# Performance work log

Measured on AMD Instinct MI355X. Metric: run time of the kernel, lower is better.

## Reference

```python
import jax, jax.numpy as jnp
import numpy as np
import math

B, S, D, H, R, DFF = 4, 1024, 1024, 16, 64, 4096

def _layernorm(x, g, b, eps=1e-5):
    m = jnp.mean(x, axis=-1, keepdims=True)
    v = jnp.var(x, axis=-1, keepdims=True)
    return (x - m) / jnp.sqrt(v + eps) * g + b

def setup_inputs() -> dict:
    key = jax.random.key(0)
    ks = jax.random.split(key, 12)
    sc = 0.02
    return {
        "src": jax.random.normal(ks[0], (B, S, D), jnp.float32),
        "in_proj_w": jax.random.normal(ks[1], (3 * D, D), jnp.float32) * sc,
        "in_proj_b": jnp.zeros((3 * D,), jnp.float32),
        "out_proj_w": jax.random.normal(ks[2], (D, D), jnp.float32) * sc,
        "out_proj_b": jnp.zeros((D,), jnp.float32),
        "Qp_w": jax.random.normal(ks[3], (R, D), jnp.float32) * sc,
        "Qp_b": jnp.zeros((R,), jnp.float32),
        "Kp_w": jax.random.normal(ks[4], (R, D), jnp.float32) * sc,
        "Kp_b": jnp.zeros((R,), jnp.float32),
        "Vp_w": jax.random.normal(ks[5], (D, D), jnp.float32) * sc,
        "Vp_b": jnp.zeros((D,), jnp.float32),
        "lam": jnp.float32(0.5),
        "ff1_w": jax.random.normal(ks[6], (DFF, D), jnp.float32) * sc,
        "ff1_b": jnp.zeros((DFF,), jnp.float32),
        "ff2_w": jax.random.normal(ks[7], (D, DFF), jnp.float32) * sc,
        "ff2_b": jnp.zeros((D,), jnp.float32),
        "ln1_g": jnp.ones((D,), jnp.float32),
        "ln1_b": jnp.zeros((D,), jnp.float32),
        "ln2_g": jnp.ones((D,), jnp.float32),
        "ln2_b": jnp.zeros((D,), jnp.float32),
    }

def reference(src, in_proj_w, in_proj_b, out_proj_w, out_proj_b,
              Qp_w, Qp_b, Kp_w, Kp_b, Vp_w, Vp_b, lam,
              ff1_w, ff1_b, ff2_w, ff2_b, ln1_g, ln1_b, ln2_g, ln2_b):
    b, s, d = src.shape
    dh = d // H
    # ---- dense multi-head attention (torch nn.MultiheadAttention, eval) ----
    qkv = src @ in_proj_w.T + in_proj_b            # [B,S,3D]
    q, k, v = jnp.split(qkv, 3, axis=-1)
    q = q.reshape(b, s, H, dh).transpose(0, 2, 1, 3)  # [B,H,S,dh]
    k = k.reshape(b, s, H, dh).transpose(0, 2, 1, 3)
    v = v.reshape(b, s, H, dh).transpose(0, 2, 1, 3)
    scores = jnp.einsum('bhqd,bhkd->bhqk', q, k) / math.sqrt(dh)
    attn = jax.nn.softmax(scores, axis=-1)
    ctx = jnp.einsum('bhqk,bhkd->bhqd', attn, v)
    ctx = ctx.transpose(0, 2, 1, 3).reshape(b, s, d)
    dense_output = ctx @ out_proj_w.T + out_proj_b
    # ---- low-rank top-k sparse attention ----
    Q = src @ Qp_w.T + Qp_b                        # [B,S,R]
    K = src @ Kp_w.T + Kp_b
    V = src @ Vp_w.T + Vp_b                        # [B,S,D]
    QK = jnp.einsum('bqr,bkr->bqk', Q, K) / math.sqrt(R)
    aw = jax.nn.softmax(QK, axis=-1)               # [B,S,S]
    kk = max(1, int(s * 0.2))
    topv, topi = jax.lax.top_k(aw, kk)             # [B,S,kk]
    bi = jnp.arange(b)[:, None, None]
    si = jnp.arange(s)[None, :, None]
    sparse_attn = jnp.zeros_like(aw).at[bi, si, topi].set(topv)
    sparse_attn = sparse_attn / (jnp.sum(sparse_attn, axis=-1, keepdims=True) + 1e-9)
    sparse_output = jnp.einsum('bqk,bkd->bqd', sparse_attn, V)
    # ---- fuse, residual, norm, FFN ----
    sig = jax.nn.sigmoid(lam)
    fused = sig * dense_output + (1.0 - sig) * sparse_output
    x = _layernorm(src + fused, ln1_g, ln1_b)
    ff = jax.nn.relu(x @ ff1_w.T + ff1_b) @ ff2_w.T + ff2_b
    return _layernorm(x + ff, ln2_g, ln2_b)
```

## Files before the change

### kernel.cpp

```cpp
#include <hip/hip_runtime.h>
#include <hip/hip_bf16.h>
#include <math.h>
#include <type_traits>

typedef __hip_bfloat16 bf16;
typedef __attribute__((ext_vector_type(8))) short short8;
typedef __attribute__((ext_vector_type(4))) float f32x4;

#define NB 4
#define NS 1024
#define ND 1024
#define NH 16
#define NDH 64
#define NR 64
#define NDFF 4096
#define NM (NB*NS)
#define NTOPK 204

static __device__ __forceinline__ float b2f(bf16 x) { return __bfloat162float(x); }
static __device__ __forceinline__ bf16  f2b(float x) { return __float2bfloat16(x); }
static __device__ __forceinline__ unsigned short bfbits(float x) {
  bf16 h = __float2bfloat16(x);
  return *reinterpret_cast<unsigned short*>(&h);
}

static __device__ __forceinline__ void gload_lds16(const void* g, void* l) {
  __builtin_amdgcn_global_load_lds(
      (const __attribute__((address_space(1))) void*)g,
      (__attribute__((address_space(3))) void*)l, 16, 0, 0);
}

template<int N> static __device__ __forceinline__ void vm_wait() {
  if constexpr (N == 0)       asm volatile("s_waitcnt vmcnt(0)" ::: "memory");
  else if constexpr (N == 2)  asm volatile("s_waitcnt vmcnt(2)" ::: "memory");
  else if constexpr (N == 4)  asm volatile("s_waitcnt vmcnt(4)" ::: "memory");
  else if constexpr (N == 6)  asm volatile("s_waitcnt vmcnt(6)" ::: "memory");
  else if constexpr (N == 8)  asm volatile("s_waitcnt vmcnt(8)" ::: "memory");
  else static_assert(N == 0, "unsupported vmcnt");
}
static __device__ __forceinline__ void bar() {
  asm volatile("s_barrier" ::: "memory");
}

static __device__ __forceinline__ void ld8(const bf16* p, float* d) {
  const uint4 u = *(const uint4*)p;
  d[0] = __uint_as_float((u.x & 0xffffu) << 16);
  d[1] = __uint_as_float(u.x & 0xffff0000u);
  d[2] = __uint_as_float((u.y & 0xffffu) << 16);
  d[3] = __uint_as_float(u.y & 0xffff0000u);
  d[4] = __uint_as_float((u.z & 0xffffu) << 16);
  d[5] = __uint_as_float(u.z & 0xffff0000u);
  d[6] = __uint_as_float((u.w & 0xffffu) << 16);
  d[7] = __uint_as_float(u.w & 0xffff0000u);
}

static __device__ __forceinline__ float block_sum_256(float v, float* rbuf, int tid) {
  rbuf[tid] = v;
  __syncthreads();
  #pragma unroll
  for (int st = 128; st > 0; st >>= 1) {
    if (tid < st) rbuf[tid] += rbuf[tid + st];
    __syncthreads();
  }
  const float r = rbuf[0];
  __syncthreads();
  return r;
}

struct CastArgs {
  const float* in[6];
  bf16* out[6];
  unsigned end[6];
};
__global__ __launch_bounds__(256) void cast6_kernel(CastArgs a) {
  const unsigned b = blockIdx.x;
  int r = 0; unsigned base = 0;
  #pragma unroll
  for (int k = 0; k < 5; ++k)
    if (b >= a.end[k]) { r = k + 1; base = a.end[k]; }
  const float* in = a.in[r];
  bf16* out = a.out[r];
  const unsigned i = ((b - base) * 256 + threadIdx.x) * 4;
  const float4 v = *(const float4*)(in + i);
  uint2 o;
  o.x = (unsigned)bfbits(v.x) | ((unsigned)bfbits(v.y) << 16);
  o.y = (unsigned)bfbits(v.z) | ((unsigned)bfbits(v.w) << 16);
  *(uint2*)(out + i) = o;
}

__global__ __launch_bounds__(256) void pack_w_kernel(
    const float* __restrict__ W, bf16* __restrict__ out, int K) {
  const int lane = threadIdx.x & 63, sub = threadIdx.x >> 6;
  const int kt2 = blockIdx.x * 4 + sub;
  const int nt  = blockIdx.y;
  const int lm = lane & 15, quad = lane >> 4;
  const float* p = W + (size_t)(nt * 16 + lm) * K + kt2 * 32 + quad * 8;
  const float4 a = *(const float4*)p;
  const float4 b = *(const float4*)(p + 4);
  uint4 o;
  o.x = (unsigned)bfbits(a.x) | ((unsigned)bfbits(a.y) << 16);
  o.y = (unsigned)bfbits(a.z) | ((unsigned)bfbits(a.w) << 16);
  o.z = (unsigned)bfbits(b.x) | ((unsigned)bfbits(b.y) << 16);
  o.w = (unsigned)bfbits(b.z) | ((unsigned)bfbits(b.w) << 16);
  *(uint4*)(out + (((size_t)(nt * (K >> 5) + kt2)) << 9) + lane * 8) = o;
}

__global__ __launch_bounds__(256) void pack_qk_kernel(
    const float* __restrict__ Qw, const float* __restrict__ Kw,
    const float* __restrict__ Qb, const float* __restrict__ Kb,
    bf16* __restrict__ w, float* __restrict__ bias) {
  const int r = blockIdx.x;
  const float* srcw = (r < 64) ? (Qw + (size_t)r * ND) : (Kw + (size_t)(r - 64) * ND);
  for (int i = threadIdx.x; i < ND; i += 256) w[(size_t)r * ND + i] = f2b(srcw[i]);
  if (r == 0)
    for (int i = threadIdx.x; i < 128; i += 256)
      bias[i] = (i < 64) ? Qb[i] : Kb[i - 64];
}

template<int BM, int BN, int BK, int BIAS, int RELU, int OUTF32>
__global__ __launch_bounds__(256) void mfma_gemm(
    const bf16* __restrict__ A, const bf16* __restrict__ W,
    const float* __restrict__ bias, void* __restrict__ C,
    int K, int lda, int ldb, int ldc,
    long long aHi, long long aLo, long long bHi, long long bLo,
    long long cHi, long long cLo, float scale)
{
  constexpr int WTM = BM / 2;
  constexpr int WTN = BN / 2;
  constexpr int AM = WTM / 16;
  constexpr int AN = WTN / 16;
  constexpr int KK = BK / 32;
  constexpr int SLOTS = BK / 8;
  constexpr int RPC = 512 / BK;
  constexpr int LPW = (BM * BK) / 2048 + (BN * BK) / 2048;
  __shared__ short As[2][BM * BK];
  __shared__ short Bs[2][BN * BK];
  const int tid  = threadIdx.x;
  const int lane = tid & 63;
  const int w    = tid >> 6;
  const int z    = blockIdx.z;
  const long long aOff = (long long)(z >> 4) * aHi + (long long)(z & 15) * aLo;
  const long long bOff = (long long)(z >> 4) * bHi + (long long)(z & 15) * bLo;
  const long long cOff = (long long)(z >> 4) * cHi + (long long)(z & 15) * cLo;

  int bx = blockIdx.x, by = blockIdx.y;
  if ((gridDim.x & 7) == 0) {
    const unsigned lin = blockIdx.y * gridDim.x + blockIdx.x;
    const unsigned Wd = gridDim.x >> 3;
    const unsigned xcd = lin & 7, i = lin >> 3;
    bx = (int)(xcd * Wd + (i % Wd));
    by = (int)(i / Wd);
  }
  const int m0 = by * BM;
  const int n0 = bx * BN;
  const int wr = w >> 1, wc = w & 1;
  const int lm = lane & 15, quad = lane >> 4;

  f32x4 acc[AM][AN];
  #pragma unroll
  for (int i = 0; i < AM; ++i)
    #pragma unroll
    for (int j = 0; j < AN; ++j) acc[i][j] = (f32x4){0.f, 0.f, 0.f, 0.f};

  const int slot = lane & (SLOTS - 1);
  const int sr   = lane / SLOTS;
  const int swz  = (BK == 32) ? ((sr >> 1) & 3) : (sr & 7);
  const int scol = (slot ^ swz) << 3;
  const int xv   = (BK == 32) ? ((lm >> 1) & 3) : (lm & 7);
  const bf16* Ab = A + aOff;
  const bf16* Bb = W + bOff;

  auto stage = [&](int buf, int k0) {
    #pragma unroll
    for (int t = 0; t < (BM * BK) / 2048; ++t) {
      const int row = w * (BM / 4) + t * RPC;
      gload_lds16(Ab + (long long)(m0 + row + sr) * lda + k0 + scol, &As[buf][row * BK]);
    }
    #pragma unroll
    for (int t = 0; t < (BN * BK) / 2048; ++t) {
      const int row = w * (BN / 4) + t * RPC;
      gload_lds16(Bb + (long long)(n0 + row + sr) * ldb + k0 + scol, &Bs[buf][row * BK]);
    }
  };
  auto compute = [&](int buf) {
    #pragma unroll
    for (int kk = 0; kk < KK; ++kk) {
      const int cb = ((kk * 4 + quad) ^ xv) << 3;
      short8 af[AM], bfr[AN];
      #pragma unroll
      for (int i = 0; i < AM; ++i)
        af[i] = *(const short8*)&As[buf][(wr * WTM + i * 16 + lm) * BK + cb];
      #pragma unroll
      for (int j = 0; j < AN; ++j)
        bfr[j] = *(const short8*)&Bs[buf][(wc * WTN + j * 16 + lm) * BK + cb];
      #pragma unroll
      for (int i = 0; i < AM; ++i)
        #pragma unroll
        for (int j = 0; j < AN; ++j)
          acc[i][j] = __builtin_amdgcn_mfma_f32_16x16x32_bf16(af[i], bfr[j], acc[i][j], 0, 0, 0);
    }
  };

  stage(0, 0);
  int cur = 0;
  for (int k0 = BK; k0 < K; k0 += BK) {
    stage(cur ^ 1, k0);
    vm_wait<LPW>();
    bar();
    compute(cur);
    bar();
    cur ^= 1;
  }
  vm_wait<0>();
  bar();
  compute(cur);

  #pragma unroll
  for (int i = 0; i < AM; ++i) {
    #pragma unroll
    for (int j = 0; j < AN; ++j) {
      const int n = n0 + wc * WTN + j * 16 + lm;
      const float bj = BIAS ? bias[n] : 0.f;
      #pragma unroll
      for (int rr = 0; rr < 4; ++rr) {
        const int m = m0 + wr * WTM + i * 16 + quad * 4 + rr;
        float v = acc[i][j][rr] * scale + bj;
        if (RELU) v = fmaxf(v, 0.f);
        const long long co = cOff + (long long)m * ldc + n;
        if (OUTF32) ((float*)C)[co] = v;
        else        ((bf16*)C)[co] = f2b(v);
      }
    }
  }
}

template<int BIAS, int RELU, int PACKOUT>
__global__ __launch_bounds__(256) void mfma_gemm_pb(
    const bf16* __restrict__ A, const bf16* __restrict__ Bp,
    const float* __restrict__ bias, bf16* __restrict__ C,
    int K, int lda, int ldc,
    long long aLo, long long bLo, long long cLo)
{
  __shared__ short As[2][128 * 64];
  const int tid = threadIdx.x, lane = tid & 63, w = tid >> 6;
  const int z = blockIdx.z;
  const long long aOff = (long long)z * aLo;
  const long long cOff = (long long)z * cLo;
  int bx = blockIdx.x, by = blockIdx.y;
  if ((gridDim.x & 7) == 0) {
    const unsigned lin = blockIdx.y * gridDim.x + blockIdx.x;
    const unsigned Wd = gridDim.x >> 3;
    const unsigned xcd = lin & 7, i = lin >> 3;
    bx = (int)(xcd * Wd + (i % Wd));
    by = (int)(i / Wd);
  }
  const int m0 = by * 128, n0 = bx * 64;
  const int wr = w >> 1, wc = w & 1;
  const int lm = lane & 15, quad = lane >> 4;
  const int KT2 = K >> 5;

  f32x4 acc[4][2];
  #pragma unroll
  for (int i = 0; i < 4; ++i)
    #pragma unroll
    for (int j = 0; j < 2; ++j) acc[i][j] = (f32x4){0.f, 0.f, 0.f, 0.f};

  const int slot = lane & 7, sr = lane >> 3;
  const int scol = (slot ^ sr) << 3;
  const int xv   = lm & 7;
  const bf16* Ab = A + aOff;
  const bf16* Bb = Bp + (long long)z * bLo
                 + (((long long)(n0 / 16 + wc * 2) * KT2) << 9) + lane * 8;

  auto stageA = [&](int buf, int t) {
    const int k0 = t * 64;
    #pragma unroll
    for (int u = 0; u < 4; ++u) {
      const int row = w * 32 + u * 8;
      gload_lds16(Ab + (long long)(m0 + row + sr) * lda + k0 + scol, &As[buf][row * 64]);
    }
  };
  short8 brg[2][4];
  auto loadB = [&](auto BUF, int t) {
    constexpr int bu = decltype(BUF)::value;
    #pragma unroll
    for (int j = 0; j < 2; ++j)
      #pragma unroll
      for (int kk = 0; kk < 2; ++kk)
        brg[bu][j * 2 + kk] =
            *(const short8*)(Bb + (((long long)j * KT2 + t * 2 + kk) << 9));
  };
  auto compute = [&](auto BUF) {
    constexpr int bu = decltype(BUF)::value;
    #pragma unroll
    for (int kk = 0; kk < 2; ++kk) {
      const int cb = ((kk * 4 + quad) ^ xv) << 3;
      short8 af[4];
      #pragma unroll
      for (int i = 0; i < 4; ++i)
        af[i] = *(const short8*)&As[bu][(wr * 64 + i * 16 + lm) * 64 + cb];
      #pragma unroll
      for (int i = 0; i < 4; ++i)
        #pragma unroll
        for (int j = 0; j < 2; ++j)
          acc[i][j] = __builtin_amdgcn_mfma_f32_16x16x32_bf16(
              af[i], brg[bu][j * 2 + kk], acc[i][j], 0, 0, 0);
    }
  };
  const std::integral_constant<int, 0> B0{};
  const std::integral_constant<int, 1> B1{};

  const int nt = K / 64;
  stageA(0, 0); loadB(B0, 0);
  for (int t = 1; t + 1 < nt; t += 2) {
    stageA(1, t);     loadB(B1, t);
    vm_wait<8>(); bar(); compute(B0); bar();
    stageA(0, t + 1); loadB(B0, t + 1);
    vm_wait<8>(); bar(); compute(B1); bar();
  }
  stageA(1, nt - 1); loadB(B1, nt - 1);
  vm_wait<8>(); bar(); compute(B0); bar();
  vm_wait<0>(); bar(); compute(B1);

  #pragma unroll
  for (int i = 0; i < 4; ++i) {
    #pragma unroll
    for (int j = 0; j < 2; ++j) {
      const int n = n0 + wc * 32 + j * 16 + lm;
      const float bj = BIAS ? bias[n] : 0.f;
      float v0 = acc[i][j][0] + bj;
      float v1 = acc[i][j][1] + bj;
      float v2 = acc[i][j][2] + bj;
      float v3 = acc[i][j][3] + bj;
      if (RELU) {
        v0 = fmaxf(v0, 0.f); v1 = fmaxf(v1, 0.f);
        v2 = fmaxf(v2, 0.f); v3 = fmaxf(v3, 0.f);
      }
      const int mm = m0 + wr * 64 + i * 16 + quad * 4;
      if (PACKOUT) {
        const int b = mm >> 10, s = mm & 1023;
        bf16* dst = C + (long long)b * ((long long)NS * ND)
                  + (((long long)(n >> 4) * (NS >> 5) + (s >> 5)) << 9)
                  + (((s >> 3) & 3) * 16 + (n & 15)) * 8 + (s & 7);
        uint2 u;
        u.x = (unsigned)bfbits(v0) | ((unsigned)bfbits(v1) << 16);
        u.y = (unsigned)bfbits(v2) | ((unsigned)bfbits(v3) << 16);
        *(uint2*)dst = u;
      } else {
        C[cOff + (long long)(mm + 0) * ldc + n] = f2b(v0);
        C[cOff + (long long)(mm + 1) * ldc + n] = f2b(v1);
        C[cOff + (long long)(mm + 2) * ldc + n] = f2b(v2);
        C[cOff + (long long)(mm + 3) * ldc + n] = f2b(v3);
      }
    }
  }
}

template<int BIAS, int RELU, int VT>
__global__ __launch_bounds__(512) void mfma_gemm256(
    const bf16* __restrict__ A, const bf16* __restrict__ W,
    const float* __restrict__ bias, bf16* __restrict__ C,
    int K, int lda, int ldb, int ldc, bf16* __restrict__ C2)
{
  __shared__ short As[2][256 * 64];
  __shared__ short Bs[2][256 * 64];
  const int tid  = threadIdx.x;
  const int lane = tid & 63;
  const int w    = tid >> 6;
  int bx = blockIdx.x, by = blockIdx.y;
  if ((gridDim.x & 7) == 0) {
    const unsigned lin = blockIdx.y * gridDim.x + blockIdx.x;
    const unsigned Wd = gridDim.x >> 3;
    const unsigned xcd = lin & 7, i = lin >> 3;
    bx = (int)(xcd * Wd + (i % Wd));
    by = (int)(i / Wd);
  }
  const int m0 = by * 256;
  const int n0 = bx * 256;
  const int wr = w >> 2, wc = w & 3;
  const int lm = lane & 15, quad = lane >> 4;

  f32x4 acc[8][4];
  #pragma unroll
  for (int i = 0; i < 8; ++i)
    #pragma unroll
    for (int j = 0; j < 4; ++j) acc[i][j] = (f32x4){0.f, 0.f, 0.f, 0.f};

  const int slot = lane & 7, sr = lane >> 3;
  const int scol = (slot ^ sr) << 3;
  const int xv   = lm & 7;

  auto stgA = [&](int buf, int c, int k0) {
    gload_lds16(A + (long long)(m0 + c * 64 + w * 8 + sr) * lda + k0 + scol,
                &As[buf][(c * 64 + w * 8) * 64]);
  };
  auto stgB = [&](int buf, int c, int k0) {
    gload_lds16(W + (long long)(n0 + c * 64 + w * 8 + sr) * ldb + k0 + scol,
                &Bs[buf][(c * 64 + w * 8) * 64]);
  };
  auto dsA = [&](short8* afr, int h, int buf) {
    #pragma unroll
    for (int i = 0; i < 4; ++i)
      #pragma unroll
      for (int kk = 0; kk < 2; ++kk)
        afr[i * 2 + kk] = *(const short8*)
            &As[buf][(wr * 128 + h * 64 + i * 16 + lm) * 64 + (((kk * 4 + quad) ^ xv) << 3)];
  };
  auto dsB = [&](short8* bfr, int jh, int buf) {
    #pragma unroll
    for (int j = 0; j < 2; ++j)
      #pragma unroll
      for (int kk = 0; kk < 2; ++kk)
        bfr[j * 2 + kk] = *(const short8*)
            &Bs[buf][(wc * 64 + jh * 32 + j * 16 + lm) * 64 + (((kk * 4 + quad) ^ xv) << 3)];
  };
  auto mmaq = [&](auto H, auto JH, const short8* afr, const short8* bfr) {
    constexpr int h = decltype(H)::value, jh = decltype(JH)::value;
    __builtin_amdgcn_s_setprio(1);
    #pragma unroll
    for (int i = 0; i < 4; ++i)
      #pragma unroll
      for (int j = 0; j < 2; ++j)
        #pragma unroll
        for (int kk = 0; kk < 2; ++kk)
          acc[h * 4 + i][jh * 2 + j] = __builtin_amdgcn_mfma_f32_16x16x32_bf16(
              afr[i * 2 + kk], bfr[j * 2 + kk], acc[h * 4 + i][jh * 2 + j], 0, 0, 0);
    __builtin_amdgcn_s_setprio(0);
  };
  const std::integral_constant<int, 0> C0{};
  const std::integral_constant<int, 1> C1{};

  stgB(0, 0, 0); stgB(0, 1, 0); stgB(0, 2, 0); stgB(0, 3, 0);
  stgA(0, 0, 0); stgA(0, 2, 0); stgA(0, 1, 0); stgA(0, 3, 0);
  vm_wait<0>();
  bar();

  const int NT = K / 64;
  int p = 0;
  for (int kt = 0; kt < NT; ++kt, p ^= 1) {
    const int k1 = (kt + 1) * 64;
    const bool pre = (kt + 1 < NT);
    short8 afr[8], bfrA[4], bfrB[4];
    dsA(afr, 0, p); dsB(bfrA, 0, p);
    if (pre) { stgB(p ^ 1, 0, k1); stgB(p ^ 1, 1, k1); }
    bar();
    mmaq(C0, C0, afr, bfrA);
    bar();
    dsB(bfrB, 1, p);
    if (pre) { stgB(p ^ 1, 2, k1); stgB(p ^ 1, 3, k1); vm_wait<4>(); }
    else vm_wait<0>();
    bar();
    mmaq(C0, C1, afr, bfrB);
    bar();
    dsA(afr, 1, p);
    if (pre) { stgA(p ^ 1, 0, k1); stgA(p ^ 1, 2, k1); }
    bar();
    mmaq(C1, C0, afr, bfrA);
    bar();
    if (pre) { stgA(p ^ 1, 1, k1); stgA(p ^ 1, 3, k1); vm_wait<2>(); }
    else vm_wait<0>();
    bar();
    mmaq(C1, C1, afr, bfrB);
    bar();
  }

  #pragma unroll
  for (int i = 0; i < 8; ++i) {
    #pragma unroll
    for (int j = 0; j < 4; ++j) {
      const int n = n0 + wc * 64 + j * 16 + lm;
      const float bj = BIAS ? bias[n] : 0.f;
      float v0 = acc[i][j][0] + bj;
      float v1 = acc[i][j][1] + bj;
      float v2 = acc[i][j][2] + bj;
      float v3 = acc[i][j][3] + bj;
      if (RELU) {
        v0 = fmaxf(v0, 0.f); v1 = fmaxf(v1, 0.f);
        v2 = fmaxf(v2, 0.f); v3 = fmaxf(v3, 0.f);
      }
      const int mm = m0 + wr * 128 + i * 16 + quad * 4;
      if (VT && n0 >= 2 * ND) {
        const int h = (n - 2 * ND) >> 6, d = (n - 2 * ND) & 63;
        uint2 u;
        u.x = (unsigned)bfbits(v0) | ((unsigned)bfbits(v1) << 16);
        u.y = (unsigned)bfbits(v2) | ((unsigned)bfbits(v3) << 16);
        bf16* dst = C2 + (long long)((mm >> 10) * NH + h) * (NDH * NS)
                       + (long long)d * NS + (mm & 1023);
        *(uint2*)dst = u;
      } else {
        C[(long long)(mm + 0) * ldc + n] = f2b(v0);
        C[(long long)(mm + 1) * ldc + n] = f2b(v1);
        C[(long long)(mm + 2) * ldc + n] = f2b(v2);
        C[(long long)(mm + 3) * ldc + n] = f2b(v3);
      }
    }
  }
}

__global__ __launch_bounds__(256) void attn_kernel(
    const bf16* __restrict__ qkv,
    const bf16* __restrict__ Vt,
    bf16* __restrict__ ctx)
{
  __shared__ short smem[2][2][64 * 64];
  const int tid = threadIdx.x, lane = tid & 63, w = tid >> 6;
  const int lm = lane & 15, quad = lane >> 4;
  const int z = blockIdx.y, b = z >> 4, h = z & 15;
  const int q0 = blockIdx.x * 128;
  const bf16* Qb = qkv + (long long)b * NS * 3072 + h * 64;
  const bf16* Kb = Qb + ND;
  const bf16* Vb = Vt + (long long)z * (NDH * NS);

  short8 qf[2][2];
  #pragma unroll
  for (int j = 0; j < 2; ++j)
    #pragma unroll
    for (int kk = 0; kk < 2; ++kk)
      qf[j][kk] = *(const short8*)(Qb + (long long)(q0 + w * 32 + j * 16 + lm) * 3072
                                      + kk * 32 + quad * 8);

  const int slot = lane & 7, sr = lane >> 3;
  const int scol = (slot ^ sr) << 3;

  auto stage = [&](int buf, int t) {
    #pragma unroll
    for (int u = 0; u < 2; ++u) {
      const int row = w * 16 + u * 8;
      gload_lds16(Kb + (long long)(t * 64 + row + sr) * 3072 + scol,
                  &smem[buf][0][row * 64]);
    }
    #pragma unroll
    for (int u = 0; u < 2; ++u) {
      const int row = w * 16 + u * 8;
      gload_lds16(Vb + (long long)(row + sr) * NS + t * 64 + scol,
                  &smem[buf][1][row * 64]);
    }
  };

  f32x4 o[4][2];
  #pragma unroll
  for (int i = 0; i < 4; ++i)
    #pragma unroll
    for (int j = 0; j < 2; ++j) o[i][j] = (f32x4){0.f, 0.f, 0.f, 0.f};
  float l[2] = {0.f, 0.f};

  stage(0, 0);
  for (int t = 0; t < 16; ++t) {
    const int buf = t & 1;
    if (t < 15) { stage(buf ^ 1, t + 1); vm_wait<4>(); }
    else        { vm_wait<0>(); }
    bar();

    f32x4 st[4][2];
    #pragma unroll
    for (int i = 0; i < 4; ++i)
      #pragma unroll
      for (int j = 0; j < 2; ++j) st[i][j] = (f32x4){0.f, 0.f, 0.f, 0.f};
    #pragma unroll
    for (int kk = 0; kk < 2; ++kk) {
      const int cb = ((kk * 4 + quad) ^ (lm & 7)) << 3;
      short8 ka[4];
      #pragma unroll
      for (int i = 0; i < 4; ++i)
        ka[i] = *(const short8*)&smem[buf][0][(i * 16 + lm) * 64 + cb];
      #pragma unroll
      for (int i = 0; i < 4; ++i)
        #pragma unroll
        for (int j = 0; j < 2; ++j)
          st[i][j] = __builtin_amdgcn_mfma_f32_16x16x32_bf16(ka[i], qf[j][kk], st[i][j], 0, 0, 0);
    }

    #pragma unroll
    for (int j = 0; j < 2; ++j)
      #pragma unroll
      for (int i = 0; i < 4; ++i)
        #pragma unroll
        for (int r = 0; r < 4; ++r) {
          const float e = __expf(st[i][j][r] * 0.125f);
          st[i][j][r] = e;
          l[j] += e;
        }

    unsigned u0[4][2], u1[4][2];
    #pragma unroll
    for (int i = 0; i < 4; ++i)
      #pragma unroll
      for (int j = 0; j < 2; ++j) {
        u0[i][j] = (unsigned)bfbits(st[i][j][0]) | ((unsigned)bfbits(st[i][j][1]) << 16);
        u1[i][j] = (unsigned)bfbits(st[i][j][2]) | ((unsigned)bfbits(st[i][j][3]) << 16);
      }
    const int s0l = ((quad & 1) * 2) * 16 + lm;
    const int s1l = s0l + 16;
    const bool hi = (quad >> 1) != 0;

    #pragma unroll
    for (int kk = 0; kk < 2; ++kk) {
      short8 pf[2];
      #pragma unroll
      for (int j = 0; j < 2; ++j) {
        const unsigned a0 = __shfl(u0[kk * 2][j],     s0l, 64);
        const unsigned a1 = __shfl(u1[kk * 2][j],     s0l, 64);
        const unsigned b0 = __shfl(u0[kk * 2 + 1][j], s0l, 64);
        const unsigned b1 = __shfl(u1[kk * 2 + 1][j], s0l, 64);
        const unsigned c0 = __shfl(u0[kk * 2][j],     s1l, 64);
        const unsigned c1 = __shfl(u1[kk * 2][j],     s1l, 64);
        const unsigned d0 = __shfl(u0[kk * 2 + 1][j], s1l, 64);
        const unsigned d1 = __shfl(u1[kk * 2 + 1][j], s1l, 64);
        union { uint4 u; short8 s; } cv;
        cv.u.x = hi ? b0 : a0; cv.u.y = hi ? b1 : a1;
        cv.u.z = hi ? d0 : c0; cv.u.w = hi ? d1 : c1;
        pf[j] = cv.s;
      }
      const int cb = ((kk * 4 + quad) ^ (lm & 7)) << 3;
      short8 va[4];
      #pragma unroll
      for (int i = 0; i < 4; ++i)
        va[i] = *(const short8*)&smem[buf][1][(i * 16 + lm) * 64 + cb];
      #pragma unroll
      for (int i = 0; i < 4; ++i)
        #pragma unroll
        for (int j = 0; j < 2; ++j)
          o[i][j] = __builtin_amdgcn_mfma_f32_16x16x32_bf16(va[i], pf[j], o[i][j], 0, 0, 0);
    }
    bar();
  }

  short (*OL)[72] = (short(*)[72])&smem[0][0][0];
  #pragma unroll
  for (int j = 0; j < 2; ++j) {
    float lj = l[j];
    lj += __shfl_xor(lj, 16, 64);
    lj += __shfl_xor(lj, 32, 64);
    const float inv = 1.f / lj;
    #pragma unroll
    for (int i = 0; i < 4; ++i) {
      uint2 u;
      u.x = (unsigned)bfbits(o[i][j][0] * inv) | ((unsigned)bfbits(o[i][j][1] * inv) << 16);
      u.y = (unsigned)bfbits(o[i][j][2] * inv) | ((unsigned)bfbits(o[i][j][3] * inv) << 16);
      *(uint2*)&OL[w * 32 + j * 16 + lm][i * 16 + quad * 4] = u;
    }
  }
  __syncthreads();
  {
    const int q = tid >> 1, c = (tid & 1) * 32;
    const uint4 r0 = *(const uint4*)&OL[q][c];
    const uint4 r1 = *(const uint4*)&OL[q][c + 8];
    const uint4 r2 = *(const uint4*)&OL[q][c + 16];
    const uint4 r3 = *(const uint4*)&OL[q][c + 24];
    bf16* dst = ctx + ((long long)(b * NS + q0 + q)) * 1024 + h * 64 + c;
    ((uint4*)dst)[0] = r0; ((uint4*)dst)[1] = r1;
    ((uint4*)dst)[2] = r2; ((uint4*)dst)[3] = r3;
  }
}

__global__ __launch_bounds__(256) void sparse_select_kernel(
    const float* __restrict__ S, bf16* __restrict__ aw)
{
  __shared__ unsigned hist[4][256];
  const int tid = threadIdx.x;
  const int lane = tid & 63;
  const int wv = tid >> 6;
  const long long row = (long long)blockIdx.x * 4 + wv;

  float sv[16];
  const float* sp = S + row * 1024 + lane * 16;
  #pragma unroll
  for (int c = 0; c < 4; ++c) {
    const float4 v = ((const float4*)sp)[c];
    sv[4*c] = v.x; sv[4*c+1] = v.y; sv[4*c+2] = v.z; sv[4*c+3] = v.w;
  }
  unsigned key[16];
  #pragma unroll
  for (int j = 0; j < 16; ++j) {
    const unsigned u = __float_as_uint(sv[j]);
    key[j] = (u & 0x80000000u) ? ~u : (u | 0x80000000u);
  }

  unsigned pref = 0u;
  int need = NTOPK;
  #pragma unroll
  for (int p = 3; p >= 0; --p) {
    *(uint4*)&hist[wv][lane * 4] = (uint4){0u, 0u, 0u, 0u};
    __syncthreads();
    const int sh = (p + 1) * 8;
    #pragma unroll
    for (int j = 0; j < 16; ++j) {
      const bool part = (p == 3) || ((key[j] >> sh) == pref);
      if (part) atomicAdd(&hist[wv][(key[j] >> (p * 8)) & 255u], 1u);
    }
    __syncthreads();
    const unsigned h0 = hist[wv][4*lane],     h1 = hist[wv][4*lane + 1];
    const unsigned h2 = hist[wv][4*lane + 2], h3 = hist[wv][4*lane + 3];
    const unsigned s3 = h3, s2 = h2 + s3, s1 = h1 + s2, s0 = h0 + s1;
    unsigned sum = s0;
    #pragma unroll
    for (int d2 = 1; d2 < 64; d2 <<= 1) {
      const unsigned t = __shfl_down(sum, d2, 64);
      if (lane < 64 - d2) sum += t;
    }
    const unsigned above = sum - s0;
    const unsigned cum[4]  = {above + s0, above + s1, above + s2, above + s3};
    const unsigned next[4] = {above + s1, above + s2, above + s3, above};
    unsigned candPref = 0u; int candNeed = 0; bool has = false;
    #pragma unroll
    for (int i = 0; i < 4; ++i) {
      if ((int)cum[i] >= need && (int)next[i] < need) {
        has = true;
        candPref = (pref << 8) | (unsigned)(4 * lane + i);
        candNeed = need - (int)next[i];
      }
    }
    const unsigned long long m = __ballot(has);
    const int srcLane = (int)(__ffsll((long long)m) - 1);
    pref = (unsigned)__shfl((int)candPref, srcLane, 64);
    need = __shfl(candNeed, srcLane, 64);
  }

  const unsigned T = pref;
  const unsigned tb = (T & 0x80000000u) ? (T ^ 0x80000000u) : ~T;
  const float thr = __uint_as_float(tb);

  float wvv[16];
  float psTop = 0.f, psAll = 0.f;
  #pragma unroll
  for (int j = 0; j < 16; ++j) {
    const float e = __expf(sv[j] - thr);
    psAll += e;
    const float wt = (key[j] >= T) ? e : 0.f;
    psTop += wt;
    wvv[j] = wt;
  }
  #pragma unroll
  for (int s = 1; s < 64; s <<= 1) {
    psTop += __shfl_xor(psTop, s, 64);
    psAll += __shfl_xor(psAll, s, 64);
  }
  const float inv = 1.f / (psTop + 1e-9f * psAll);

  uint4 o0, o1;
  o0.x = (unsigned)bfbits(wvv[0]*inv)  | ((unsigned)bfbits(wvv[1]*inv)  << 16);
  o0.y = (unsigned)bfbits(wvv[2]*inv)  | ((unsigned)bfbits(wvv[3]*inv)  << 16);
  o0.z = (unsigned)bfbits(wvv[4]*inv)  | ((unsigned)bfbits(wvv[5]*inv)  << 16);
  o0.w = (unsigned)bfbits(wvv[6]*inv)  | ((unsigned)bfbits(wvv[7]*inv)  << 16);
  o1.x = (unsigned)bfbits(wvv[8]*inv)  | ((unsigned)bfbits(wvv[9]*inv)  << 16);
  o1.y = (unsigned)bfbits(wvv[10]*inv) | ((unsigned)bfbits(wvv[11]*inv) << 16);
  o1.z = (unsigned)bfbits(wvv[12]*inv) | ((unsigned)bfbits(wvv[13]*inv) << 16);
  o1.w = (unsigned)bfbits(wvv[14]*inv) | ((unsigned)bfbits(wvv[15]*inv) << 16);
  bf16* op = aw + row * 1024 + lane * 16;
  ((uint4*)op)[0] = o0; ((uint4*)op)[1] = o1;
}

__global__ __launch_bounds__(256) void fuse_ln1_kernel(
    const float* __restrict__ src, const bf16* __restrict__ dense,
    const bf16* __restrict__ sparse, const float* __restrict__ lam,
    const float* __restrict__ g, const float* __restrict__ beta,
    bf16* __restrict__ x1)
{
  __shared__ float y[ND];
  __shared__ float rbuf[256];
  const int tid = threadIdx.x;
  const size_t base = (size_t)blockIdx.x * ND;
  const float sig = 1.f / (1.f + __expf(-lam[0]));
  const float c1 = 1.f - sig;
  float s1 = 0.f, s2 = 0.f;
  #pragma unroll
  for (int j = 0; j < 4; ++j) {
    const int i = tid + (j << 8);
    const float v = src[base + i] + sig * b2f(dense[base + i]) + c1 * b2f(sparse[base + i]);
    y[i] = v; s1 += v; s2 += v * v;
  }
  const float sum1 = block_sum_256(s1, rbuf, tid);
  const float sum2 = block_sum_256(s2, rbuf, tid);
  const float mean = sum1 * (1.f / ND);
  const float var  = sum2 * (1.f / ND) - mean * mean;
  const float rstd = rsqrtf(var + 1e-5f);
  #pragma unroll
  for (int j = 0; j < 4; ++j) {
    const int i = tid + (j << 8);
    x1[base + i] = f2b((y[i] - mean) * rstd * g[i] + beta[i]);
  }
}

__global__ __launch_bounds__(256) void ln2_kernel(
    const bf16* __restrict__ x1, const bf16* __restrict__ ff,
    const float* __restrict__ g, const float* __restrict__ beta,
    float* __restrict__ outp)
{
  __shared__ float y[ND];
  __shared__ float rbuf[256];
  const int tid = threadIdx.x;
  const size_t base = (size_t)blockIdx.x * ND;
  float s1 = 0.f, s2 = 0.f;
  #pragma unroll
  for (int j = 0; j < 4; ++j) {
    const int i = tid + (j << 8);
    const float v = b2f(x1[base + i]) + b2f(ff[base + i]);
    y[i] = v; s1 += v; s2 += v * v;
  }
  const float sum1 = block_sum_256(s1, rbuf, tid);
  const float sum2 = block_sum_256(s2, rbuf, tid);
  const float mean = sum1 * (1.f / ND);
  const float var  = sum2 * (1.f / ND) - mean * mean;
  const float rstd = rsqrtf(var + 1e-5f);
  #pragma unroll
  for (int j = 0; j < 4; ++j) {
    const int i = tid + (j << 8);
    outp[base + i] = (y[i] - mean) * rstd * g[i] + beta[i];
  }
}

extern "C" void kernel_launch(void* const* d_in, const int* in_sizes, int n_in,
                              void* d_out, int out_size, void* d_ws, size_t ws_size,
                              hipStream_t stream)
{
  const float* src        = (const float*)d_in[0];
  const float* in_proj_w  = (const float*)d_in[1];
  const float* in_proj_b  = (const float*)d_in[2];
  const float* out_proj_w = (const float*)d_in[3];
  const float* out_proj_b = (const float*)d_in[4];
  const float* Qp_w  = (const float*)d_in[5];
  const float* Qp_b  = (const float*)d_in[6];
  const float* Kp_w  = (const float*)d_in[7];
  const float* Kp_b  = (const float*)d_in[8];
  const float* Vp_w  = (const float*)d_in[9];
  const float* Vp_b  = (const float*)d_in[10];
  const float* lam   = (const float*)d_in[11];
  const float* ff1_w = (const float*)d_in[12];
  const float* ff1_b = (const float*)d_in[13];
  const float* ff2_w = (const float*)d_in[14];
  const float* ff2_b = (const float*)d_in[15];
  const float* ln1_g = (const float*)d_in[16];
  const float* ln1_b = (const float*)d_in[17];
  const float* ln2_g = (const float*)d_in[18];
  const float* ln2_b = (const float*)d_in[19];
  (void)in_sizes; (void)n_in; (void)out_size; (void)ws_size;

  char* ws = (char*)d_ws;
  size_t off = 0;
  auto take = [&](size_t bytes) -> void* {
    void* p = ws + off; off += (bytes + 255) & ~(size_t)255; return p;
  };
  bf16*  src_bf  = (bf16*) take((size_t)NM * ND * 2);
  bf16*  w_qkv   = (bf16*) take((size_t)3 * ND * ND * 2);
  bf16*  w_out_p = (bf16*) take((size_t)ND * ND * 2);
  bf16*  w_vp_p  = (bf16*) take((size_t)ND * ND * 2);
  bf16*  w_ff1   = (bf16*) take((size_t)NDFF * ND * 2);
  bf16*  w_ff2_p = (bf16*) take((size_t)ND * NDFF * 2);
  bf16*  w_qk    = (bf16*) take((size_t)128 * ND * 2);
  float* bias_qk = (float*)take(128 * 4);
  const size_t mark = off;
  bf16*  qkv     = (bf16*) take((size_t)NM * 3 * ND * 2);
  bf16*  Vt_all  = (bf16*) take((size_t)NH * NS * NS * 2);
  bf16*  Vt_old  = (bf16*) take((size_t)NH * NDH * NS * 2);
  bf16*  ctx     = (bf16*) take((size_t)NM * ND * 2);
  bf16*  dense   = (bf16*) take((size_t)NM * ND * 2);
  bf16*  QKs_bf  = (bf16*) take((size_t)NM * 128 * 2);
  bf16*  Vsp     = (bf16*) take((size_t)NM * ND * 2);
  bf16*  sparse  = (bf16*) take((size_t)NM * ND * 2);
  (void)Vt_old; (void)Vsp;
  bf16*  x1    = (bf16*)(ws + mark);
  bf16*  h1    = (bf16*)(ws + mark + (size_t)NM * ND * 2);
  bf16*  ffout = (bf16*)(ws + mark + (size_t)NM * ND * 2 + (size_t)NM * NDFF * 2);
  bf16*  aw    = (bf16*)(ws + mark + 2 * (size_t)NM * ND * 2 + (size_t)NM * NDFF * 2);
  float* S_sp  = (float*)(ws + mark + (size_t)NM * ND * 2);
  bf16*  Vsp_pk = (bf16*)ctx;

  const dim3 blk(256);
  bf16* const NOC2 = nullptr;
  {
    CastArgs a;
    a.in[0] = src;        a.out[0] = src_bf;
    a.in[1] = in_proj_w;  a.out[1] = w_qkv;
    a.in[2] = ff1_w;      a.out[2] = w_ff1;
    a.in[3] = src;        a.out[3] = src_bf;
    a.in[4] = src;        a.out[4] = src_bf;
    a.in[5] = src;        a.out[5] = src_bf;
    a.end[0] = 4096; a.end[1] = 7168; a.end[2] = 11264;
    a.end[3] = 11264; a.end[4] = 11264; a.end[5] = 11264;
    cast6_kernel<<<dim3(11264), blk, 0, stream>>>(a);
  }
  pack_w_kernel<<<dim3(ND/128,   ND/16), blk, 0, stream>>>(out_proj_w, w_out_p, ND);
  pack_w_kernel<<<dim3(ND/128,   ND/16), blk, 0, stream>>>(Vp_w,       w_vp_p,  ND);
  pack_w_kernel<<<dim3(NDFF/128, ND/16), blk, 0, stream>>>(ff2_w,      w_ff2_p, NDFF);
  pack_qk_kernel<<<dim3(128), blk, 0, stream>>>(Qp_w, Kp_w, Qp_b, Kp_b, w_qk, bias_qk);

  mfma_gemm256<1,0,1><<<dim3(3*ND/256, NM/256), dim3(512), 0, stream>>>(
      src_bf, w_qkv, in_proj_b, qkv, ND, ND, ND, 3*ND, Vt_all);

  attn_kernel<<<dim3(NS/128, NB*NH), blk, 0, stream>>>(qkv, Vt_all, ctx);

  mfma_gemm_pb<1,0,0><<<dim3(ND/64, NM/128, 1), blk, 0, stream>>>(
      ctx, w_out_p, out_proj_b, dense, ND, ND, ND, 0, 0, 0);
  mfma_gemm<128,64,64,1,0,0><<<dim3(2, NM/128, 1), blk, 0, stream>>>(
      src_bf, w_qk, bias_qk, QKs_bf, ND, ND, ND, 128, 0,0, 0,0, 0,0, 1.f);
  mfma_gemm<128,64,64,0,0,1><<<dim3(NS/64, NS/128, NB), blk, 0, stream>>>(
      QKs_bf, QKs_bf + 64, nullptr, S_sp, 64, 128, 128, NS,
      0, (long long)NS*128, 0, (long long)NS*128, 0, (long long)NS*NS, 0.125f);
  mfma_gemm_pb<1,0,1><<<dim3(ND/64, NM/128, 1), blk, 0, stream>>>(
      src_bf, w_vp_p, Vp_b, Vsp_pk, ND, ND, 0, 0, 0, 0);
  sparse_select_kernel<<<dim3(NM/4), blk, 0, stream>>>(S_sp, aw);
  mfma_gemm_pb<0,0,0><<<dim3(ND/64, NS/128, NB), blk, 0, stream>>>(
      aw, Vsp_pk, nullptr, sparse, NS, NS, ND,
      (long long)NS*ND, (long long)NS*ND, (long long)NS*ND);
  fuse_ln1_kernel<<<dim3(NM), blk, 0, stream>>>(src, dense, sparse, lam, ln1_g, ln1_b, x1);
  mfma_gemm256<1,1,0><<<dim3(NDFF/256, NM/256), dim3(512), 0, stream>>>(
      x1, w_ff1, ff1_b, h1, ND, ND, ND, NDFF, NOC2);
  mfma_gemm_pb<1,0,0><<<dim3(ND/64, NM/128, 1), blk, 0, stream>>>(
      h1, w_ff2_p, ff2_b, ffout, NDFF, NDFF, ND, 0, 0, 0);
  ln2_kernel<<<dim3(NM), blk, 0, stream>>>(x1, ffout, ln2_g, ln2_b, (float*)d_out);
}
```

Before: 413.8 us.

## Write GEMM A-operands in MFMA-packed layout and add LDS-free packed GEMM

The producers of the A operands (attention ctx, sparse top-k weights, FF1 output) now write directly in a 16x32 MFMA fragment-packed layout. A new LDS-free GEMM kernel then loads both operands straight from global memory into registers with double buffering, using 128x128 tiles. It replaces the earlier packed-B GEMM for out_proj, the sparse AV product and FF2. This removes LDS staging and barriers, but the producers now issue scattered narrow stores and the GEMM depends on L2/cache reuse instead of shared memory.

```diff
diff --git a/kernel.cpp b/kernel.cpp
--- a/kernel.cpp
+++ b/kernel.cpp
@@ -40,18 +40,6 @@
 }
 static __device__ __forceinline__ void bar() {
   asm volatile("s_barrier" ::: "memory");
-}
-
-static __device__ __forceinline__ void ld8(const bf16* p, float* d) {
-  const uint4 u = *(const uint4*)p;
-  d[0] = __uint_as_float((u.x & 0xffffu) << 16);
-  d[1] = __uint_as_float(u.x & 0xffff0000u);
-  d[2] = __uint_as_float((u.y & 0xffffu) << 16);
-  d[3] = __uint_as_float(u.y & 0xffff0000u);
-  d[4] = __uint_as_float((u.z & 0xffffu) << 16);
-  d[5] = __uint_as_float(u.z & 0xffff0000u);
-  d[6] = __uint_as_float((u.w & 0xffffu) << 16);
-  d[7] = __uint_as_float(u.w & 0xffff0000u);
 }
 
 static __device__ __forceinline__ float block_sum_256(float v, float* rbuf, int tid) {
@@ -356,7 +344,75 @@
   }
 }
 
-template<int BIAS, int RELU, int VT>
+template<int BIAS>
+__global__ __launch_bounds__(256) void mfma_gemm_np(
+    const bf16* __restrict__ Ap, const bf16* __restrict__ Bp,
+    const float* __restrict__ bias, bf16* __restrict__ C,
+    int K, int ldc, long long bLo)
+{
+  const int tid = threadIdx.x, lane = tid & 63, w = tid >> 6;
+  const int wr = w >> 1, wc = w & 1;
+  const int lm = lane & 15, quad = lane >> 4;
+  const int m0 = blockIdx.y * 128, n0 = blockIdx.x * 128;
+  const int KT2 = K >> 5;
+  const long long bOff = (long long)(m0 >> 10) * bLo;
+
+  f32x4 acc[4][4];
+  #pragma unroll
+  for (int i = 0; i < 4; ++i)
+    #pragma unroll
+    for (int j = 0; j < 4; ++j) acc[i][j] = (f32x4){0.f, 0.f, 0.f, 0.f};
+
+  const bf16* Abase = Ap + (((long long)((m0 >> 4) + wr * 4) * KT2) << 9) + lane * 8;
+  const bf16* Bbase = Bp + bOff
+                    + (((long long)((n0 >> 4) + wc * 4) * KT2) << 9) + lane * 8;
+
+  short8 ar[2][4], br[2][4];
+  auto loadT = [&](auto BUF, int kt2) {
+    constexpr int bu = decltype(BUF)::value;
+    #pragma unroll
+    for (int i = 0; i < 4; ++i)
+      ar[bu][i] = *(const short8*)(Abase + (((long long)i * KT2 + kt2) << 9));
+    #pragma unroll
+    for (int j = 0; j < 4; ++j)
+      br[bu][j] = *(const short8*)(Bbase + (((long long)j * KT2 + kt2) << 9));
+  };
+  auto computeT = [&](auto BUF) {
+    constexpr int bu = decltype(BUF)::value;
+    #pragma unroll
+    for (int i = 0; i < 4; ++i)
+      #pragma unroll
+      for (int j = 0; j < 4; ++j)
+        acc[i][j] = __builtin_amdgcn_mfma_f32_16x16x32_bf16(
+            ar[bu][i], br[bu][j], acc[i][j], 0, 0, 0);
+  };
+  const std::integral_constant<int, 0> B0{};
+  const std::integral_constant<int, 1> B1{};
+
+  loadT(B0, 0);
+  for (int t = 1; t + 1 < KT2; t += 2) {
+    loadT(B1, t);     vm_wait<8>(); computeT(B0);
+    loadT(B0, t + 1); vm_wait<8>(); computeT(B1);
+  }
+  loadT(B1, KT2 - 1); vm_wait<8>(); computeT(B0);
+  vm_wait<0>(); computeT(B1);
+
+  #pragma unroll
+  for (int i = 0; i < 4; ++i) {
+    #pragma unroll
+    for (int j = 0; j < 4; ++j) {
+      const int n = n0 + wc * 64 + j * 16 + lm;
+      const float bj = BIAS ? bias[n] : 0.f;
+      const int mm = m0 + wr * 64 + i * 16 + quad * 4;
+      C[(long long)(mm + 0) * ldc + n] = f2b(acc[i][j][0] + bj);
+      C[(long long)(mm + 1) * ldc + n] = f2b(acc[i][j][1] + bj);
+      C[(long long)(mm + 2) * ldc + n] = f2b(acc[i][j][2] + bj);
+      C[(long long)(mm + 3) * ldc + n] = f2b(acc[i][j][3] + bj);
+    }
+  }
+}
+
+template<int BIAS, int RELU, int VT, int PACKA>
 __global__ __launch_bounds__(512) void mfma_gemm256(
     const bf16* __restrict__ A, const bf16* __restrict__ W,
     const float* __restrict__ bias, bf16* __restrict__ C,
@@ -487,6 +543,13 @@
         bf16* dst = C2 + (long long)((mm >> 10) * NH + h) * (NDH * NS)
                        + (long long)d * NS + (mm & 1023);
         *(uint2*)dst = u;
+      } else if (PACKA) {
+        const long long blk = (long long)(mm >> 4) * (ldc >> 5) + (n >> 5);
+        bf16* base = C + (blk << 9) + ((n >> 3) & 3) * 128 + (n & 7) + (mm & 15) * 8;
+        base[0]  = f2b(v0);
+        base[8]  = f2b(v1);
+        base[16] = f2b(v2);
+        base[24] = f2b(v3);
       } else {
         C[(long long)(mm + 0) * ldc + n] = f2b(v0);
         C[(long long)(mm + 1) * ldc + n] = f2b(v1);
@@ -647,9 +710,14 @@
     const uint4 r1 = *(const uint4*)&OL[q][c + 8];
     const uint4 r2 = *(const uint4*)&OL[q][c + 16];
     const uint4 r3 = *(const uint4*)&OL[q][c + 24];
-    bf16* dst = ctx + ((long long)(b * NS + q0 + q)) * 1024 + h * 64 + c;
-    ((uint4*)dst)[0] = r0; ((uint4*)dst)[1] = r1;
-    ((uint4*)dst)[2] = r2; ((uint4*)dst)[3] = r3;
+    const int row = b * NS + q0 + q;
+    const int k = h * 64 + c;
+    const long long blk = (long long)(row >> 4) * 32 + (k >> 5);
+    bf16* base = ctx + (blk << 9) + (row & 15) * 8;
+    *(uint4*)(base)       = r0;
+    *(uint4*)(base + 128) = r1;
+    *(uint4*)(base + 256) = r2;
+    *(uint4*)(base + 384) = r3;
   }
 }
 
@@ -746,8 +814,10 @@
   o1.y = (unsigned)bfbits(wvv[10]*inv) | ((unsigned)bfbits(wvv[11]*inv) << 16);
   o1.z = (unsigned)bfbits(wvv[12]*inv) | ((unsigned)bfbits(wvv[13]*inv) << 16);
   o1.w = (unsigned)bfbits(wvv[14]*inv) | ((unsigned)bfbits(wvv[15]*inv) << 16);
-  bf16* op = aw + row * 1024 + lane * 16;
-  ((uint4*)op)[0] = o0; ((uint4*)op)[1] = o1;
+  const long long blk = (long long)(row >> 4) * 32 + (lane >> 1);
+  bf16* op = aw + (blk << 9) + (int)(row & 15) * 8 + (lane & 1) * 256;
+  *(uint4*)(op)       = o0;
+  *(uint4*)(op + 128) = o1;
 }
 
 __global__ __launch_bounds__(256) void fuse_ln1_kernel(
@@ -884,13 +954,13 @@
   pack_w_kernel<<<dim3(NDFF/128, ND/16), blk, 0, stream>>>(ff2_w,      w_ff2_p, NDFF);
   pack_qk_kernel<<<dim3(128), blk, 0, stream>>>(Qp_w, Kp_w, Qp_b, Kp_b, w_qk, bias_qk);
 
-  mfma_gemm256<1,0,1><<<dim3(3*ND/256, NM/256), dim3(512), 0, stream>>>(
+  mfma_gemm256<1,0,1,0><<<dim3(3*ND/256, NM/256), dim3(512), 0, stream>>>(
       src_bf, w_qkv, in_proj_b, qkv, ND, ND, ND, 3*ND, Vt_all);
 
   attn_kernel<<<dim3(NS/128, NB*NH), blk, 0, stream>>>(qkv, Vt_all, ctx);
 
-  mfma_gemm_pb<1,0,0><<<dim3(ND/64, NM/128, 1), blk, 0, stream>>>(
-      ctx, w_out_p, out_proj_b, dense, ND, ND, ND, 0, 0, 0);
+  mfma_gemm_np<1><<<dim3(ND/128, NM/128), blk, 0, stream>>>(
+      ctx, w_out_p, out_proj_b, dense, ND, ND, 0);
   mfma_gemm<128,64,64,1,0,0><<<dim3(2, NM/128, 1), blk, 0, stream>>>(
       src_bf, w_qk, bias_qk, QKs_bf, ND, ND, ND, 128, 0,0, 0,0, 0,0, 1.f);
   mfma_gemm<128,64,64,0,0,1><<<dim3(NS/64, NS/128, NB), blk, 0, stream>>>(
@@ -899,13 +969,12 @@
   mfma_gemm_pb<1,0,1><<<dim3(ND/64, NM/128, 1), blk, 0, stream>>>(
       src_bf, w_vp_p, Vp_b, Vsp_pk, ND, ND, 0, 0, 0, 0);
   sparse_select_kernel<<<dim3(NM/4), blk, 0, stream>>>(S_sp, aw);
-  mfma_gemm_pb<0,0,0><<<dim3(ND/64, NS/128, NB), blk, 0, stream>>>(
-      aw, Vsp_pk, nullptr, sparse, NS, NS, ND,
-      (long long)NS*ND, (long long)NS*ND, (long long)NS*ND);
+  mfma_gemm_np<0><<<dim3(ND/128, NM/128), blk, 0, stream>>>(
+      aw, Vsp_pk, nullptr, sparse, NS, ND, (long long)NS*ND);
   fuse_ln1_kernel<<<dim3(NM), blk, 0, stream>>>(src, dense, sparse, lam, ln1_g, ln1_b, x1);
-  mfma_gemm256<1,1,0><<<dim3(NDFF/256, NM/256), dim3(512), 0, stream>>>(
+  mfma_gemm256<1,1,0,1><<<dim3(NDFF/256, NM/256), dim3(512), 0, stream>>>(
       x1, w_ff1, ff1_b, h1, ND, ND, ND, NDFF, NOC2);
-  mfma_gemm_pb<1,0,0><<<dim3(ND/64, NM/128, 1), blk, 0, stream>>>(
-      h1, w_ff2_p, ff2_b, ffout, NDFF, NDFF, ND, 0, 0, 0);
+  mfma_gemm_np<1><<<dim3(ND/128, NM/128), blk, 0, stream>>>(
+      h1, w_ff2_p, ff2_b, ffout, NDFF, ND, 0);
   ln2_kernel<<<dim3(NM), blk, 0, stream>>>(x1, ffout, ln2_g, ln2_b, (float*)d_out);
 }
```

Measured after the change: 461.0 us. 1.11x slower.
